# Kernel optimization log

Hardware: AMD Instinct MI355X
Metric: run time of the kernel (lower is better)

## Reference

```python
import jax, jax.numpy as jnp
import numpy as np

B, N, D = 8, 2048, 512


def setup_inputs() -> dict:
    key = jax.random.key(0)
    ks = jax.random.split(key, 5)
    bound = 1.0 / np.sqrt(D)
    return {
        "query": jax.random.normal(ks[0], (B, N, D), dtype=jnp.float32),
        "context": jax.random.normal(ks[1], (B, N, D), dtype=jnp.float32),
        "Wq": jax.random.uniform(ks[2], (D, D), minval=-bound, maxval=bound, dtype=jnp.float32),
        "bq": jnp.zeros((D,), dtype=jnp.float32),
        "Wv": jax.random.uniform(ks[3], (D, D), minval=-bound, maxval=bound, dtype=jnp.float32),
        "bv": jnp.zeros((D,), dtype=jnp.float32),
        "Wo": jax.random.uniform(ks[4], (D, D), minval=-bound, maxval=bound, dtype=jnp.float32),
        "bo": jnp.zeros((D,), dtype=jnp.float32),
    }


def reference(query, context, Wq, bq, Wv, bv, Wo, bo):
    d = query.shape[-1]
    scale = 1.0 / jnp.sqrt(jnp.asarray(d, dtype=query.dtype))
    # Linear projections (eqx.nn.Linear: y = W @ x + b -> x @ W.T + b)
    q = jnp.einsum("bnd,ed->bne", query, Wq) + bq      # (B, N, D)
    v = jnp.einsum("bnd,ed->bne", context, Wv) + bv    # (B, N, D)
    # NOTE: original module computes scores against RAW context (key layer unused)
    scores = jnp.einsum("bqd,bkd->bqk", q, context) * scale  # (B, N, N)
    attn = jax.nn.softmax(scores, axis=-1)
    h = jnp.einsum("bqk,bkd->bqd", attn, v)            # (B, N, D)
    return jnp.einsum("bnd,ed->bne", h, Wo) + bo
```

## Files before the change

kernel.cpp:

```cpp
#include <hip/hip_runtime.h>
#include <math.h>

#define NB  8
#define SEQ 2048
#define DIM 512

typedef short v8s __attribute__((ext_vector_type(8)));
typedef float v4f __attribute__((ext_vector_type(4)));

__device__ __forceinline__ unsigned short f2bf(float f) {
    unsigned int u = __float_as_uint(f);
    u += 0x7fffu + ((u >> 16) & 1u);
    return (unsigned short)(u >> 16);
}
__device__ __forceinline__ float bf2f(unsigned short h) {
    return __uint_as_float((unsigned int)h << 16);
}
__device__ __forceinline__ void async16(const unsigned short* g, unsigned short* l) {
    __builtin_amdgcn_global_load_lds(
        (const __attribute__((address_space(1))) unsigned int*)g,
        (__attribute__((address_space(3))) unsigned int*)l, 16, 0, 0);
}

__global__ __launch_bounds__(256)
void conv_bf16(const float* __restrict__ x, unsigned short* __restrict__ y)
{
    int i = blockIdx.x * 256 + threadIdx.x;
    float4 v = ((const float4*)x)[i];
    ushort4 o; o.x = f2bf(v.x); o.y = f2bf(v.y); o.z = f2bf(v.z); o.w = f2bf(v.w);
    ((ushort4*)y)[i] = o;
}

template<int MODE>
__global__ __launch_bounds__(256, 2)
void proj_sgl(const unsigned short* __restrict__ Xbf, const float* __restrict__ W,
              const float* __restrict__ bias, unsigned short* __restrict__ Y)
{
    __shared__ __align__(16) unsigned short As[128 * 64];
    __shared__ __align__(16) unsigned short Bs[128 * 64];

    const int t = threadIdx.x, wave = t >> 6, lane = t & 63;
    const int l15 = lane & 15, quad = lane >> 4;
    const int m0 = blockIdx.x * 128, e0 = blockIdx.y * 128;

    v4f hacc[2][8];
#pragma unroll
    for (int mt = 0; mt < 2; mt++)
#pragma unroll
        for (int nt = 0; nt < 8; nt++) hacc[mt][nt] = (v4f){0.f, 0.f, 0.f, 0.f};

    const int lr8 = lane >> 3, lc8 = lane & 7;

#define STAGE_A(bk)                                                            \
    _Pragma("unroll") for (int i = 0; i < 4; i++) {                            \
        int row = wave * 32 + i * 8 + lr8;                                     \
        int lc = lc8 ^ (row & 7);                                              \
        async16(Xbf + (size_t)(m0 + row) * DIM + (bk) * 64 + lc * 8,           \
                &As[(wave * 32 + i * 8) * 64]);                                \
    }
#define STAGE_B(bk)                                                            \
    _Pragma("unroll") for (int j = 0; j < 8; j++) {                            \
        int u = t * 8 + j;                                                     \
        int row = u >> 4, c4 = u & 15;                                         \
        float4 wv = *(const float4*)(W + (size_t)(e0 + row) * DIM + (bk) * 64 + c4 * 4); \
        ushort4 o = make_ushort4(f2bf(wv.x), f2bf(wv.y), f2bf(wv.z), f2bf(wv.w)); \
        int sc = (c4 >> 1) ^ (row & 7);                                        \
        *(ushort4*)&Bs[row * 64 + sc * 8 + (c4 & 1) * 4] = o;                  \
    }

    STAGE_A(0) STAGE_B(0)
    for (int bk = 0; bk < 8; bk++) {
        __syncthreads();
#pragma unroll
        for (int kc = 0; kc < 2; kc++) {
            v8s a[2];
#pragma unroll
            for (int mt = 0; mt < 2; mt++) {
                int row = wave * 32 + mt * 16 + l15;
                a[mt] = *(const v8s*)&As[row * 64 + (((kc * 4 + quad) ^ (row & 7)) * 8)];
            }
#pragma unroll
            for (int nt = 0; nt < 8; nt++) {
                int er = nt * 16 + l15;
                v8s bfr = *(const v8s*)&Bs[er * 64 + (((kc * 4 + quad) ^ (er & 7)) * 8)];
#pragma unroll
                for (int mt = 0; mt < 2; mt++)
                    hacc[mt][nt] = __builtin_amdgcn_mfma_f32_16x16x32_bf16(a[mt], bfr, hacc[mt][nt], 0, 0, 0);
            }
        }
        __syncthreads();
        if (bk + 1 < 8) { STAGE_A(bk + 1) STAGE_B(bk + 1) }
    }
#undef STAGE_A
#undef STAGE_B

#pragma unroll
    for (int mt = 0; mt < 2; mt++)
#pragma unroll
        for (int nt = 0; nt < 8; nt++) {
            int col = e0 + nt * 16 + l15;
            float bb = bias[col];
            if (MODE == 0) {
#pragma unroll
                for (int r = 0; r < 4; r++) {
                    int row = m0 + wave * 32 + mt * 16 + quad * 4 + r;
                    Y[(size_t)row * DIM + col] = f2bf(hacc[mt][nt][r] + bb);
                }
            } else {
                int rowb = m0 + wave * 32 + mt * 16 + quad * 4;
                int bidx = rowb >> 11, n = rowb & 2047;
                ushort4 o = make_ushort4(f2bf(hacc[mt][nt][0] + bb), f2bf(hacc[mt][nt][1] + bb),
                                         f2bf(hacc[mt][nt][2] + bb), f2bf(hacc[mt][nt][3] + bb));
                *(ushort4*)&Y[(size_t)bidx * DIM * SEQ + (size_t)col * SEQ + n] = o;
            }
        }
}

__global__ __launch_bounds__(256, 2)
void proj_split(const unsigned short* __restrict__ Ahi, const unsigned short* __restrict__ Alo,
                const float* __restrict__ W, const float* __restrict__ bias,
                float* __restrict__ Y)
{
    __shared__ __align__(16) unsigned short Ah[128 * 64];
    __shared__ __align__(16) unsigned short Al[128 * 64];
    __shared__ __align__(16) unsigned short Bh[128 * 64];
    __shared__ __align__(16) unsigned short Bl[128 * 64];

    const int t = threadIdx.x, wave = t >> 6, lane = t & 63;
    const int l15 = lane & 15, quad = lane >> 4;
    const int m0 = blockIdx.x * 128, e0 = blockIdx.y * 128;

    v4f hacc[2][8];
#pragma unroll
    for (int mt = 0; mt < 2; mt++)
#pragma unroll
        for (int nt = 0; nt < 8; nt++) hacc[mt][nt] = (v4f){0.f, 0.f, 0.f, 0.f};

    const int lr8 = lane >> 3, lc8 = lane & 7;

#define STAGE_A2(bk)                                                           \
    _Pragma("unroll") for (int i = 0; i < 4; i++) {                            \
        int row = wave * 32 + i * 8 + lr8;                                     \
        int lc = lc8 ^ (row & 7);                                              \
        size_t ga = (size_t)(m0 + row) * DIM + (bk) * 64 + lc * 8;             \
        async16(Ahi + ga, &Ah[(wave * 32 + i * 8) * 64]);                      \
        async16(Alo + ga, &Al[(wave * 32 + i * 8) * 64]);                      \
    }
#define STAGE_B2(bk)                                                           \
    _Pragma("unroll") for (int j = 0; j < 8; j++) {                            \
        int u = t * 8 + j;                                                     \
        int row = u >> 4, c4 = u & 15;                                         \
        float4 wv = *(const float4*)(W + (size_t)(e0 + row) * DIM + (bk) * 64 + c4 * 4); \
        ushort4 oh = make_ushort4(f2bf(wv.x), f2bf(wv.y), f2bf(wv.z), f2bf(wv.w)); \
        ushort4 ol = make_ushort4(f2bf(wv.x - bf2f(oh.x)), f2bf(wv.y - bf2f(oh.y)), \
                                  f2bf(wv.z - bf2f(oh.z)), f2bf(wv.w - bf2f(oh.w))); \
        int sc = (c4 >> 1) ^ (row & 7);                                        \
        int sa = row * 64 + sc * 8 + (c4 & 1) * 4;                             \
        *(ushort4*)&Bh[sa] = oh;                                               \
        *(ushort4*)&Bl[sa] = ol;                                               \
    }

    STAGE_A2(0) STAGE_B2(0)
    for (int bk = 0; bk < 8; bk++) {
        __syncthreads();
#pragma unroll
        for (int kc = 0; kc < 2; kc++) {
            v8s ah[2], al[2];
#pragma unroll
            for (int mt = 0; mt < 2; mt++) {
                int row = wave * 32 + mt * 16 + l15;
                int sa = row * 64 + (((kc * 4 + quad) ^ (row & 7)) * 8);
                ah[mt] = *(const v8s*)&Ah[sa];
                al[mt] = *(const v8s*)&Al[sa];
            }
#pragma unroll
            for (int nt = 0; nt < 8; nt++) {
                int er = nt * 16 + l15;
                int sb = er * 64 + (((kc * 4 + quad) ^ (er & 7)) * 8);
                v8s bh = *(const v8s*)&Bh[sb];
                v8s bl = *(const v8s*)&Bl[sb];
#pragma unroll
                for (int mt = 0; mt < 2; mt++) {
                    hacc[mt][nt] = __builtin_amdgcn_mfma_f32_16x16x32_bf16(ah[mt], bh, hacc[mt][nt], 0, 0, 0);
                    hacc[mt][nt] = __builtin_amdgcn_mfma_f32_16x16x32_bf16(al[mt], bh, hacc[mt][nt], 0, 0, 0);
                    hacc[mt][nt] = __builtin_amdgcn_mfma_f32_16x16x32_bf16(ah[mt], bl, hacc[mt][nt], 0, 0, 0);
                }
            }
        }
        __syncthreads();
        if (bk + 1 < 8) { STAGE_A2(bk + 1) STAGE_B2(bk + 1) }
    }
#undef STAGE_A2
#undef STAGE_B2

#pragma unroll
    for (int mt = 0; mt < 2; mt++)
#pragma unroll
        for (int nt = 0; nt < 8; nt++) {
            int col = e0 + nt * 16 + l15;
            float bb = bias[col];
#pragma unroll
            for (int r = 0; r < 4; r++) {
                int row = m0 + wave * 32 + mt * 16 + quad * 4 + r;
                Y[(size_t)row * DIM + col] = hacc[mt][nt][r] + bb;
            }
        }
}

__global__ __launch_bounds__(512, 2)
void flash_mfma2(const unsigned short* __restrict__ qbf,
                 const unsigned short* __restrict__ ctxbf,
                 const unsigned short* __restrict__ vT,
                 unsigned short* __restrict__ hhi,
                 unsigned short* __restrict__ hlo)
{
    __shared__ __align__(16) unsigned short Ks[64 * 512];
    __shared__ __align__(16) unsigned short Ps[64 * 72];
    __shared__ __align__(16) float Sf[64 * 68];
    __shared__ float alphaS[64];

    const int t = threadIdx.x;
    const int wave = t >> 6, lane = t & 63;
    const int l15 = lane & 15, quad = lane >> 4;
    const int strip = wave & 3, half = wave >> 2;
    const int lr = lane >> 3, l8 = lane & 7;
    const int b = blockIdx.y, m0 = blockIdx.x * 64;

    const unsigned short* ctxb = ctxbf + (size_t)b * SEQ * DIM;
    const unsigned short* vTb  = vT    + (size_t)b * DIM * SEQ;
    const float scale = 0.044194173824159216f;

    v8s qf[16];
    {
        const unsigned short* qrow = qbf + ((size_t)b * SEQ + m0 + strip * 16 + l15) * DIM;
#pragma unroll
        for (int kc = 0; kc < 16; kc++)
            qf[kc] = *(const v8s*)(qrow + kc * 32 + quad * 8);
    }
    v4f hacc[4][4];
#pragma unroll
    for (int m = 0; m < 4; m++)
#pragma unroll
        for (int dt = 0; dt < 4; dt++) hacc[m][dt] = (v4f){0.f, 0.f, 0.f, 0.f};

    float M = -INFINITY, L = 0.f;

#pragma unroll
    for (int i = 0; i < 8; i++) {
        int row = wave * 8 + i;
        async16(ctxb + (size_t)row * DIM + (size_t)(lane ^ (row & 7)) * 8, &Ks[row * 512]);
    }

    for (int kt = 0; kt < SEQ / 64; kt++) {
        __syncthreads();
        v8s vf[4][2];
#pragma unroll
        for (int dt = 0; dt < 4; dt++)
#pragma unroll
            for (int kc = 0; kc < 2; kc++)
                vf[dt][kc] = *(const v8s*)(vTb + (size_t)(wave * 64 + dt * 16 + l15) * SEQ
                                           + kt * 64 + kc * 32 + quad * 8);
        v4f sacc[2];
        sacc[0] = (v4f){0.f, 0.f, 0.f, 0.f};
        sacc[1] = (v4f){0.f, 0.f, 0.f, 0.f};
#pragma unroll
        for (int kc = 0; kc < 16; kc++) {
#pragma unroll
            for (int ct = 0; ct < 2; ct++) {
                int key = half * 32 + ct * 16 + l15;
                v8s kf = *(const v8s*)&Ks[key * 512 + (((kc * 4 + quad) ^ (key & 7)) * 8)];
                sacc[ct] = __builtin_amdgcn_mfma_f32_16x16x32_bf16(qf[kc], kf, sacc[ct], 0, 0, 0);
            }
        }
#pragma unroll
        for (int ct = 0; ct < 2; ct++)
#pragma unroll
            for (int r = 0; r < 4; r++)
                Sf[(strip * 16 + quad * 4 + r) * 68 + half * 32 + ct * 16 + l15] = sacc[ct][r] * scale;
        __syncthreads();
        {
            int row = wave * 8 + lr;
            float sv[8];
            *(float4*)&sv[0] = *(const float4*)&Sf[row * 68 + l8 * 8];
            *(float4*)&sv[4] = *(const float4*)&Sf[row * 68 + l8 * 8 + 4];
            float mx = sv[0];
#pragma unroll
            for (int j = 1; j < 8; j++) mx = fmaxf(mx, sv[j]);
#pragma unroll
            for (int off = 1; off < 8; off <<= 1) mx = fmaxf(mx, __shfl_xor(mx, off, 64));
            float Mn = fmaxf(M, mx);
            float al = __expf(M - Mn);
            float sm = 0.f;
            v8s pv;
#pragma unroll
            for (int j = 0; j < 8; j++) {
                float p = __expf(sv[j] - Mn);
                sm += p;
                pv[j] = (short)f2bf(p);
            }
#pragma unroll
            for (int off = 1; off < 8; off <<= 1) sm += __shfl_xor(sm, off, 64);
            L = L * al + sm;
            M = Mn;
            *(v8s*)&Ps[row * 72 + l8 * 8] = pv;
            if (l8 == 0) alphaS[row] = al;
        }
        __syncthreads();
        if (kt + 1 < SEQ / 64) {
#pragma unroll
            for (int i = 0; i < 8; i++) {
                int row = wave * 8 + i;
                async16(ctxb + (size_t)((kt + 1) * 64 + row) * DIM + (size_t)(lane ^ (row & 7)) * 8,
                        &Ks[row * 512]);
            }
        }
#pragma unroll
        for (int m = 0; m < 4; m++) {
            v4f a4;
#pragma unroll
            for (int r = 0; r < 4; r++) a4[r] = alphaS[m * 16 + quad * 4 + r];
#pragma unroll
            for (int dt = 0; dt < 4; dt++) hacc[m][dt] *= a4;
        }
#pragma unroll
        for (int kc = 0; kc < 2; kc++) {
            v8s pa[4];
#pragma unroll
            for (int m = 0; m < 4; m++)
                pa[m] = *(const v8s*)&Ps[(m * 16 + l15) * 72 + kc * 32 + quad * 8];
#pragma unroll
            for (int dt = 0; dt < 4; dt++)
#pragma unroll
                for (int m = 0; m < 4; m++)
                    hacc[m][dt] = __builtin_amdgcn_mfma_f32_16x16x32_bf16(pa[m], vf[dt][kc], hacc[m][dt], 0, 0, 0);
        }
    }

    __syncthreads();
    if (l8 == 0) alphaS[wave * 8 + lr] = 1.0f / L;
    __syncthreads();
#pragma unroll
    for (int m = 0; m < 4; m++) {
#pragma unroll
        for (int r = 0; r < 4; r++) {
            float invL = alphaS[m * 16 + quad * 4 + r];
            int grow = m0 + m * 16 + quad * 4 + r;
#pragma unroll
            for (int dt = 0; dt < 4; dt++) {
                float o = hacc[m][dt][r] * invL;
                unsigned short hi = f2bf(o);
                float lof = o - bf2f(hi);
                size_t idx = ((size_t)b * SEQ + grow) * DIM + wave * 64 + dt * 16 + l15;
                hhi[idx] = hi;
                hlo[idx] = f2bf(lof);
            }
        }
    }
}

extern "C" void kernel_launch(void* const* d_in, const int* in_sizes, int n_in,
                              void* d_out, int out_size, void* d_ws, size_t ws_size,
                              hipStream_t stream)
{
    const float* query   = (const float*)d_in[0];
    const float* context = (const float*)d_in[1];
    const float* Wq      = (const float*)d_in[2];
    const float* bq      = (const float*)d_in[3];
    const float* Wv      = (const float*)d_in[4];
    const float* bv      = (const float*)d_in[5];
    const float* Wo      = (const float*)d_in[6];
    const float* bo      = (const float*)d_in[7];

    const size_t NE = (size_t)NB * SEQ * DIM;
    unsigned short* qbf = (unsigned short*)d_ws;
    unsigned short* cbf = qbf + NE;
    unsigned short* hhi = cbf + NE;
    unsigned short* hlo = hhi + NE;
    unsigned short* vTb = (unsigned short*)d_out;
    unsigned short* qx  = ((unsigned short*)d_out) + NE;

    dim3 gridP(128, 4);

    conv_bf16   <<<NE / 1024, 256, 0, stream>>>(query, qx);
    conv_bf16   <<<NE / 1024, 256, 0, stream>>>(context, cbf);
    proj_sgl<0> <<<gridP, 256, 0, stream>>>(qx,  Wq, bq, qbf);
    proj_sgl<1> <<<gridP, 256, 0, stream>>>(cbf, Wv, bv, vTb);
    flash_mfma2 <<<dim3(SEQ / 64, NB), 512, 0, stream>>>(qbf, cbf, vTb, hhi, hlo);
    proj_split  <<<gridP, 256, 0, stream>>>(hhi, hlo, Wo, bo, (float*)d_out);
}
```

Baseline: 346.0 us.

## Fuse bf16 conversion into Q/V projection and rebuild flash kernel with double-buffered K

The separate fp32-to-bf16 conversion kernels are removed. The Q and V projections now read fp32 inputs directly, convert them while staging into shared memory, and run as one launch using a z grid dimension. One column of V blocks also writes the bf16 context copy as a side output. The attention kernel is rewritten to double-buffer the K tile, compute the softmax in registers with per-wave LDS flag handshakes instead of block-wide barriers and an fp32 score buffer, and use a flat 256-block grid with batch interleaving. In exchange, occupancy drops to one block per CU because LDS use grows, and the spin-wait flags rely on LDS ordering.

```diff
diff --git a/kernel.cpp b/kernel.cpp
--- a/kernel.cpp
+++ b/kernel.cpp
@@ -21,24 +21,34 @@
         (const __attribute__((address_space(1))) unsigned int*)g,
         (__attribute__((address_space(3))) unsigned int*)l, 16, 0, 0);
 }
-
-__global__ __launch_bounds__(256)
-void conv_bf16(const float* __restrict__ x, unsigned short* __restrict__ y)
-{
-    int i = blockIdx.x * 256 + threadIdx.x;
-    float4 v = ((const float4*)x)[i];
-    ushort4 o; o.x = f2bf(v.x); o.y = f2bf(v.y); o.z = f2bf(v.z); o.w = f2bf(v.w);
-    ((ushort4*)y)[i] = o;
-}
-
-template<int MODE>
+__device__ __forceinline__ void lds_fence() {
+    __builtin_amdgcn_s_waitcnt(0xc07f);
+    asm volatile("" ::: "memory");
+}
+__device__ __forceinline__ void flag_store(int* f, int v) {
+    __hip_atomic_store(f, v, __ATOMIC_RELAXED, __HIP_MEMORY_SCOPE_WORKGROUP);
+}
+__device__ __forceinline__ void flag_wait(int* f, int v) {
+    while (__hip_atomic_load(f, __ATOMIC_RELAXED, __HIP_MEMORY_SCOPE_WORKGROUP) < v) {}
+    asm volatile("" ::: "memory");
+}
+
 __global__ __launch_bounds__(256, 2)
-void proj_sgl(const unsigned short* __restrict__ Xbf, const float* __restrict__ W,
-              const float* __restrict__ bias, unsigned short* __restrict__ Y)
+void proj_qv(const float* __restrict__ query, const float* __restrict__ context,
+             const float* __restrict__ Wq, const float* __restrict__ bq,
+             const float* __restrict__ Wv, const float* __restrict__ bv,
+             unsigned short* __restrict__ qbf, unsigned short* __restrict__ vT,
+             unsigned short* __restrict__ cbf)
 {
     __shared__ __align__(16) unsigned short As[128 * 64];
     __shared__ __align__(16) unsigned short Bs[128 * 64];
 
+    const int z = blockIdx.z;
+    const float* X    = z ? context : query;
+    const float* W    = z ? Wv : Wq;
+    const float* bias = z ? bv : bq;
+    const bool   sidew = (z == 1) && (blockIdx.y == 0);
+
     const int t = threadIdx.x, wave = t >> 6, lane = t & 63;
     const int l15 = lane & 15, quad = lane >> 4;
     const int m0 = blockIdx.x * 128, e0 = blockIdx.y * 128;
@@ -49,26 +59,21 @@
 #pragma unroll
         for (int nt = 0; nt < 8; nt++) hacc[mt][nt] = (v4f){0.f, 0.f, 0.f, 0.f};
 
-    const int lr8 = lane >> 3, lc8 = lane & 7;
-
-#define STAGE_A(bk)                                                            \
-    _Pragma("unroll") for (int i = 0; i < 4; i++) {                            \
-        int row = wave * 32 + i * 8 + lr8;                                     \
-        int lc = lc8 ^ (row & 7);                                              \
-        async16(Xbf + (size_t)(m0 + row) * DIM + (bk) * 64 + lc * 8,           \
-                &As[(wave * 32 + i * 8) * 64]);                                \
-    }
-#define STAGE_B(bk)                                                            \
+#define STAGE_QV(bk)                                                           \
     _Pragma("unroll") for (int j = 0; j < 8; j++) {                            \
         int u = t * 8 + j;                                                     \
         int row = u >> 4, c4 = u & 15;                                         \
+        int sc = (c4 >> 1) ^ (row & 7);                                        \
+        float4 xv = *(const float4*)(X + (size_t)(m0 + row) * DIM + (bk) * 64 + c4 * 4); \
+        ushort4 ox = make_ushort4(f2bf(xv.x), f2bf(xv.y), f2bf(xv.z), f2bf(xv.w)); \
+        *(ushort4*)&As[row * 64 + sc * 8 + (c4 & 1) * 4] = ox;                 \
+        if (sidew) *(ushort4*)&cbf[(size_t)(m0 + row) * DIM + (bk) * 64 + c4 * 4] = ox; \
         float4 wv = *(const float4*)(W + (size_t)(e0 + row) * DIM + (bk) * 64 + c4 * 4); \
-        ushort4 o = make_ushort4(f2bf(wv.x), f2bf(wv.y), f2bf(wv.z), f2bf(wv.w)); \
-        int sc = (c4 >> 1) ^ (row & 7);                                        \
-        *(ushort4*)&Bs[row * 64 + sc * 8 + (c4 & 1) * 4] = o;                  \
-    }
-
-    STAGE_A(0) STAGE_B(0)
+        ushort4 ow = make_ushort4(f2bf(wv.x), f2bf(wv.y), f2bf(wv.z), f2bf(wv.w)); \
+        *(ushort4*)&Bs[row * 64 + sc * 8 + (c4 & 1) * 4] = ow;                 \
+    }
+
+    STAGE_QV(0)
     for (int bk = 0; bk < 8; bk++) {
         __syncthreads();
 #pragma unroll
@@ -89,10 +94,9 @@
             }
         }
         __syncthreads();
-        if (bk + 1 < 8) { STAGE_A(bk + 1) STAGE_B(bk + 1) }
-    }
-#undef STAGE_A
-#undef STAGE_B
+        if (bk + 1 < 8) { STAGE_QV(bk + 1) }
+    }
+#undef STAGE_QV
 
 #pragma unroll
     for (int mt = 0; mt < 2; mt++)
@@ -100,20 +104,183 @@
         for (int nt = 0; nt < 8; nt++) {
             int col = e0 + nt * 16 + l15;
             float bb = bias[col];
-            if (MODE == 0) {
+            if (z == 0) {
 #pragma unroll
                 for (int r = 0; r < 4; r++) {
                     int row = m0 + wave * 32 + mt * 16 + quad * 4 + r;
-                    Y[(size_t)row * DIM + col] = f2bf(hacc[mt][nt][r] + bb);
+                    qbf[(size_t)row * DIM + col] = f2bf(hacc[mt][nt][r] + bb);
                 }
             } else {
                 int rowb = m0 + wave * 32 + mt * 16 + quad * 4;
                 int bidx = rowb >> 11, n = rowb & 2047;
                 ushort4 o = make_ushort4(f2bf(hacc[mt][nt][0] + bb), f2bf(hacc[mt][nt][1] + bb),
                                          f2bf(hacc[mt][nt][2] + bb), f2bf(hacc[mt][nt][3] + bb));
-                *(ushort4*)&Y[(size_t)bidx * DIM * SEQ + (size_t)col * SEQ + n] = o;
-            }
-        }
+                *(ushort4*)&vT[(size_t)bidx * DIM * SEQ + (size_t)col * SEQ + n] = o;
+            }
+        }
+}
+
+__global__ __launch_bounds__(512, 1)
+void flash3(const unsigned short* __restrict__ qbf,
+            const unsigned short* __restrict__ cbf,
+            const unsigned short* __restrict__ vT,
+            unsigned short* __restrict__ hhi,
+            unsigned short* __restrict__ hlo)
+{
+    __shared__ __align__(16) unsigned short Ks[2][64 * 512];
+    __shared__ __align__(16) unsigned short Ps[64 * 72];
+    __shared__ float Mpart[2][64];
+    __shared__ float alphaS[64];
+    __shared__ float LL[2][64];
+    __shared__ int   flagM[8], flagP[8];
+
+    const int t = threadIdx.x, wave = t >> 6, lane = t & 63;
+    const int l15 = lane & 15, quad = lane >> 4;
+    const int strip = wave & 3, half = wave >> 2;
+    const int gid = blockIdx.x;
+    const int b = gid & 7;
+    const int m0 = (gid >> 3) * 64;
+
+    const unsigned short* ctxb = cbf + (size_t)b * SEQ * DIM;
+    const unsigned short* vTb  = vT  + (size_t)b * DIM * SEQ;
+    const float scale = 0.044194173824159216f;
+
+    if (t < 8) { flagM[t] = 0; flagP[t] = 0; }
+
+    v8s qf[16];
+    {
+        const unsigned short* qrow = qbf + ((size_t)b * SEQ + m0 + strip * 16 + l15) * DIM;
+#pragma unroll
+        for (int kc = 0; kc < 16; kc++)
+            qf[kc] = *(const v8s*)(qrow + kc * 32 + quad * 8);
+    }
+    v4f hacc[4][4];
+#pragma unroll
+    for (int m = 0; m < 4; m++)
+#pragma unroll
+        for (int dt = 0; dt < 4; dt++) hacc[m][dt] = (v4f){0.f, 0.f, 0.f, 0.f};
+    float M[4], L[4];
+#pragma unroll
+    for (int r = 0; r < 4; r++) { M[r] = -INFINITY; L[r] = 0.f; }
+
+#pragma unroll
+    for (int i = 0; i < 8; i++) {
+        int row = wave * 8 + i;
+        async16(ctxb + (size_t)row * DIM + (size_t)(lane ^ (row & 7)) * 8, &Ks[0][row * 512]);
+    }
+
+    for (int kt = 0; kt < SEQ / 64; kt++) {
+        const int p = kt & 1;
+        __syncthreads();
+        if (kt + 1 < SEQ / 64) {
+#pragma unroll
+            for (int i = 0; i < 8; i++) {
+                int row = wave * 8 + i;
+                async16(ctxb + (size_t)((kt + 1) * 64 + row) * DIM + (size_t)(lane ^ (row & 7)) * 8,
+                        &Ks[p ^ 1][row * 512]);
+            }
+        }
+        v8s vf[4][2];
+#pragma unroll
+        for (int dt = 0; dt < 4; dt++)
+#pragma unroll
+            for (int kc = 0; kc < 2; kc++)
+                vf[dt][kc] = *(const v8s*)(vTb + (size_t)(wave * 64 + dt * 16 + l15) * SEQ
+                                           + kt * 64 + kc * 32 + quad * 8);
+        v4f sacc[2][2];
+        sacc[0][0] = sacc[0][1] = sacc[1][0] = sacc[1][1] = (v4f){0.f, 0.f, 0.f, 0.f};
+#pragma unroll
+        for (int kc = 0; kc < 16; kc++) {
+#pragma unroll
+            for (int ct = 0; ct < 2; ct++) {
+                int key = half * 32 + ct * 16 + l15;
+                v8s kf = *(const v8s*)&Ks[p][key * 512 + (((kc * 4 + quad) ^ (key & 7)) * 8)];
+                sacc[ct][kc & 1] = __builtin_amdgcn_mfma_f32_16x16x32_bf16(qf[kc], kf, sacc[ct][kc & 1], 0, 0, 0);
+            }
+        }
+        float sc0[4], sc1[4], mx[4];
+#pragma unroll
+        for (int r = 0; r < 4; r++) {
+            sc0[r] = (sacc[0][0][r] + sacc[0][1][r]) * scale;
+            sc1[r] = (sacc[1][0][r] + sacc[1][1][r]) * scale;
+            float m2 = fmaxf(sc0[r], sc1[r]);
+#pragma unroll
+            for (int off = 1; off < 16; off <<= 1)
+                m2 = fmaxf(m2, __shfl_xor(m2, off, 64));
+            mx[r] = m2;
+            if (l15 == 0) Mpart[half][strip * 16 + quad * 4 + r] = m2;
+        }
+        lds_fence();
+        if (lane == 0) flag_store(&flagM[wave], kt + 1);
+        flag_wait(&flagM[wave ^ 4], kt + 1);
+        float alr[4];
+#pragma unroll
+        for (int r = 0; r < 4; r++) {
+            int row = strip * 16 + quad * 4 + r;
+            float mo = Mpart[half ^ 1][row];
+            float Mn = fmaxf(M[r], fmaxf(mx[r], mo));
+            float al = __expf(M[r] - Mn);
+            M[r] = Mn;
+            alr[r] = al;
+            float p0 = __expf(sc0[r] - Mn), p1 = __expf(sc1[r] - Mn);
+            float rs = p0 + p1;
+#pragma unroll
+            for (int off = 1; off < 16; off <<= 1)
+                rs += __shfl_xor(rs, off, 64);
+            L[r] = L[r] * al + rs;
+            Ps[row * 72 + half * 32 + l15]      = f2bf(p0);
+            Ps[row * 72 + half * 32 + 16 + l15] = f2bf(p1);
+            if (half == 0 && l15 == 0) alphaS[row] = al;
+        }
+        lds_fence();
+        if (lane == 0) flag_store(&flagP[wave], kt + 1);
+#pragma unroll
+        for (int j = 0; j < 8; j++) flag_wait(&flagP[j], kt + 1);
+#pragma unroll
+        for (int m = 0; m < 4; m++) {
+            v4f al4 = *(const v4f*)&alphaS[m * 16 + quad * 4];
+#pragma unroll
+            for (int dt = 0; dt < 4; dt++) hacc[m][dt] *= al4;
+        }
+#pragma unroll
+        for (int kc = 0; kc < 2; kc++) {
+            v8s pa[4];
+#pragma unroll
+            for (int m = 0; m < 4; m++)
+                pa[m] = *(const v8s*)&Ps[(m * 16 + l15) * 72 + kc * 32 + quad * 8];
+#pragma unroll
+            for (int dt = 0; dt < 4; dt++)
+#pragma unroll
+                for (int m = 0; m < 4; m++)
+                    hacc[m][dt] = __builtin_amdgcn_mfma_f32_16x16x32_bf16(pa[m], vf[dt][kc], hacc[m][dt], 0, 0, 0);
+        }
+    }
+
+    if (l15 == 0) {
+#pragma unroll
+        for (int r = 0; r < 4; r++) LL[half][strip * 16 + quad * 4 + r] = L[r];
+    }
+    __syncthreads();
+#pragma unroll
+    for (int m = 0; m < 4; m++) {
+        v4f l0 = *(const v4f*)&LL[0][m * 16 + quad * 4];
+        v4f l1 = *(const v4f*)&LL[1][m * 16 + quad * 4];
+        v4f inv;
+#pragma unroll
+        for (int r = 0; r < 4; r++) inv[r] = 1.0f / (l0[r] + l1[r]);
+#pragma unroll
+        for (int dt = 0; dt < 4; dt++) {
+            v4f o = hacc[m][dt] * inv;
+#pragma unroll
+            for (int r = 0; r < 4; r++) {
+                size_t idx = ((size_t)b * SEQ + m0 + m * 16 + quad * 4 + r) * DIM
+                             + wave * 64 + dt * 16 + l15;
+                unsigned short hi = f2bf(o[r]);
+                hhi[idx] = hi;
+                hlo[idx] = f2bf(o[r] - bf2f(hi));
+            }
+        }
+    }
 }
 
 __global__ __launch_bounds__(256, 2)
@@ -207,157 +374,6 @@
         }
 }
 
-__global__ __launch_bounds__(512, 2)
-void flash_mfma2(const unsigned short* __restrict__ qbf,
-                 const unsigned short* __restrict__ ctxbf,
-                 const unsigned short* __restrict__ vT,
-                 unsigned short* __restrict__ hhi,
-                 unsigned short* __restrict__ hlo)
-{
-    __shared__ __align__(16) unsigned short Ks[64 * 512];
-    __shared__ __align__(16) unsigned short Ps[64 * 72];
-    __shared__ __align__(16) float Sf[64 * 68];
-    __shared__ float alphaS[64];
-
-    const int t = threadIdx.x;
-    const int wave = t >> 6, lane = t & 63;
-    const int l15 = lane & 15, quad = lane >> 4;
-    const int strip = wave & 3, half = wave >> 2;
-    const int lr = lane >> 3, l8 = lane & 7;
-    const int b = blockIdx.y, m0 = blockIdx.x * 64;
-
-    const unsigned short* ctxb = ctxbf + (size_t)b * SEQ * DIM;
-    const unsigned short* vTb  = vT    + (size_t)b * DIM * SEQ;
-    const float scale = 0.044194173824159216f;
-
-    v8s qf[16];
-    {
-        const unsigned short* qrow = qbf + ((size_t)b * SEQ + m0 + strip * 16 + l15) * DIM;
-#pragma unroll
-        for (int kc = 0; kc < 16; kc++)
-            qf[kc] = *(const v8s*)(qrow + kc * 32 + quad * 8);
-    }
-    v4f hacc[4][4];
-#pragma unroll
-    for (int m = 0; m < 4; m++)
-#pragma unroll
-        for (int dt = 0; dt < 4; dt++) hacc[m][dt] = (v4f){0.f, 0.f, 0.f, 0.f};
-
-    float M = -INFINITY, L = 0.f;
-
-#pragma unroll
-    for (int i = 0; i < 8; i++) {
-        int row = wave * 8 + i;
-        async16(ctxb + (size_t)row * DIM + (size_t)(lane ^ (row & 7)) * 8, &Ks[row * 512]);
-    }
-
-    for (int kt = 0; kt < SEQ / 64; kt++) {
-        __syncthreads();
-        v8s vf[4][2];
-#pragma unroll
-        for (int dt = 0; dt < 4; dt++)
-#pragma unroll
-            for (int kc = 0; kc < 2; kc++)
-                vf[dt][kc] = *(const v8s*)(vTb + (size_t)(wave * 64 + dt * 16 + l15) * SEQ
-                                           + kt * 64 + kc * 32 + quad * 8);
-        v4f sacc[2];
-        sacc[0] = (v4f){0.f, 0.f, 0.f, 0.f};
-        sacc[1] = (v4f){0.f, 0.f, 0.f, 0.f};
-#pragma unroll
-        for (int kc = 0; kc < 16; kc++) {
-#pragma unroll
-            for (int ct = 0; ct < 2; ct++) {
-                int key = half * 32 + ct * 16 + l15;
-                v8s kf = *(const v8s*)&Ks[key * 512 + (((kc * 4 + quad) ^ (key & 7)) * 8)];
-                sacc[ct] = __builtin_amdgcn_mfma_f32_16x16x32_bf16(qf[kc], kf, sacc[ct], 0, 0, 0);
-            }
-        }
-#pragma unroll
-        for (int ct = 0; ct < 2; ct++)
-#pragma unroll
-            for (int r = 0; r < 4; r++)
-                Sf[(strip * 16 + quad * 4 + r) * 68 + half * 32 + ct * 16 + l15] = sacc[ct][r] * scale;
-        __syncthreads();
-        {
-            int row = wave * 8 + lr;
-            float sv[8];
-            *(float4*)&sv[0] = *(const float4*)&Sf[row * 68 + l8 * 8];
-            *(float4*)&sv[4] = *(const float4*)&Sf[row * 68 + l8 * 8 + 4];
-            float mx = sv[0];
-#pragma unroll
-            for (int j = 1; j < 8; j++) mx = fmaxf(mx, sv[j]);
-#pragma unroll
-            for (int off = 1; off < 8; off <<= 1) mx = fmaxf(mx, __shfl_xor(mx, off, 64));
-            float Mn = fmaxf(M, mx);
-            float al = __expf(M - Mn);
-            float sm = 0.f;
-            v8s pv;
-#pragma unroll
-            for (int j = 0; j < 8; j++) {
-                float p = __expf(sv[j] - Mn);
-                sm += p;
-                pv[j] = (short)f2bf(p);
-            }
-#pragma unroll
-            for (int off = 1; off < 8; off <<= 1) sm += __shfl_xor(sm, off, 64);
-            L = L * al + sm;
-            M = Mn;
-            *(v8s*)&Ps[row * 72 + l8 * 8] = pv;
-            if (l8 == 0) alphaS[row] = al;
-        }
-        __syncthreads();
-        if (kt + 1 < SEQ / 64) {
-#pragma unroll
-            for (int i = 0; i < 8; i++) {
-                int row = wave * 8 + i;
-                async16(ctxb + (size_t)((kt + 1) * 64 + row) * DIM + (size_t)(lane ^ (row & 7)) * 8,
-                        &Ks[row * 512]);
-            }
-        }
-#pragma unroll
-        for (int m = 0; m < 4; m++) {
-            v4f a4;
-#pragma unroll
-            for (int r = 0; r < 4; r++) a4[r] = alphaS[m * 16 + quad * 4 + r];
-#pragma unroll
-            for (int dt = 0; dt < 4; dt++) hacc[m][dt] *= a4;
-        }
-#pragma unroll
-        for (int kc = 0; kc < 2; kc++) {
-            v8s pa[4];
-#pragma unroll
-            for (int m = 0; m < 4; m++)
-                pa[m] = *(const v8s*)&Ps[(m * 16 + l15) * 72 + kc * 32 + quad * 8];
-#pragma unroll
-            for (int dt = 0; dt < 4; dt++)
-#pragma unroll
-                for (int m = 0; m < 4; m++)
-                    hacc[m][dt] = __builtin_amdgcn_mfma_f32_16x16x32_bf16(pa[m], vf[dt][kc], hacc[m][dt], 0, 0, 0);
-        }
-    }
-
-    __syncthreads();
-    if (l8 == 0) alphaS[wave * 8 + lr] = 1.0f / L;
-    __syncthreads();
-#pragma unroll
-    for (int m = 0; m < 4; m++) {
-#pragma unroll
-        for (int r = 0; r < 4; r++) {
-            float invL = alphaS[m * 16 + quad * 4 + r];
-            int grow = m0 + m * 16 + quad * 4 + r;
-#pragma unroll
-            for (int dt = 0; dt < 4; dt++) {
-                float o = hacc[m][dt][r] * invL;
-                unsigned short hi = f2bf(o);
-                float lof = o - bf2f(hi);
-                size_t idx = ((size_t)b * SEQ + grow) * DIM + wave * 64 + dt * 16 + l15;
-                hhi[idx] = hi;
-                hlo[idx] = f2bf(lof);
-            }
-        }
-    }
-}
-
 extern "C" void kernel_launch(void* const* d_in, const int* in_sizes, int n_in,
                               void* d_out, int out_size, void* d_ws, size_t ws_size,
                               hipStream_t stream)
@@ -377,14 +393,9 @@
     unsigned short* hhi = cbf + NE;
     unsigned short* hlo = hhi + NE;
     unsigned short* vTb = (unsigned short*)d_out;
-    unsigned short* qx  = ((unsigned short*)d_out) + NE;
-
-    dim3 gridP(128, 4);
-
-    conv_bf16   <<<NE / 1024, 256, 0, stream>>>(query, qx);
-    conv_bf16   <<<NE / 1024, 256, 0, stream>>>(context, cbf);
-    proj_sgl<0> <<<gridP, 256, 0, stream>>>(qx,  Wq, bq, qbf);
-    proj_sgl<1> <<<gridP, 256, 0, stream>>>(cbf, Wv, bv, vTb);
-    flash_mfma2 <<<dim3(SEQ / 64, NB), 512, 0, stream>>>(qbf, cbf, vTb, hhi, hlo);
-    proj_split  <<<gridP, 256, 0, stream>>>(hhi, hlo, Wo, bo, (float*)d_out);
-}
+
+    proj_qv   <<<dim3(128, 4, 2), 256, 0, stream>>>(query, context, Wq, bq, Wv, bv,
+                                                    qbf, vTb, cbf);
+    flash3    <<<256, 512, 0, stream>>>(qbf, cbf, vTb, hhi, hlo);
+    proj_split<<<dim3(128, 4), 256, 0, stream>>>(hhi, hlo, Wo, bo, (float*)d_out);
+}
```

Result: slower. 449.6 us (+30.0%).
